# Kernel tuning notes

Hardware: AMD Instinct MI355X
Metric: run time of the kernel (lower is better)

## Reference

```python
import jax, jax.numpy as jnp
import numpy as np

EPSILON = 0.1      # init kwarg epsilon
NUM_STAB = 1e-06   # init kwarg num_stab
B, D, C = 4096, 3072, 10


def setup_inputs() -> dict:
    key = jax.random.key(0)
    k1, k2 = jax.random.split(key)
    data = jax.random.normal(k1, (B, D), dtype=jnp.float32)
    # small scale keeps softmax probs near-uniform -> rho well-conditioned
    W = jax.random.normal(k2, (D, C), dtype=jnp.float32) * 0.02
    return {"data": data, "W": W}


def _probs(logits, c):
    # output = softmax(...) * (1 - c*num_stab) + num_stab  (numerical stabilization)
    p = jax.nn.softmax(logits, axis=-1)
    return p * (1.0 - c * NUM_STAB) + NUM_STAB


def reference(data, W):
    c = W.shape[1]
    m = c - 1

    def g(x):  # x: [D] -> new_output row: [m]
        p = _probs(x @ W, c)
        s = jnp.sqrt(p)
        return 2.0 * s[:m] / (1.0 - s[m])

    # Vectorized Jacobian: replaces the m sequential autograd.grad calls.
    jac = jax.vmap(jax.jacrev(g))(data)            # [B, m, D]

    p = _probs(data @ W, c)                        # [B, C]
    s_m = jnp.sqrt(p[:, m])                        # [B]
    delta = 2.0 * jnp.arccos(jnp.sqrt(p / c).sum(axis=1))   # [B]
    rho = (2.0 * (1.0 - s_m) - p[:, :m].sum(axis=1)) / (1.0 - s_m)  # [B]
    jac_norm = jnp.sqrt(jnp.square(jac).sum(axis=(1, 2)))   # [B] Frobenius norm per sample
    reg = jax.nn.elu(jac_norm - delta / (rho * EPSILON))
    return reg.mean()
```

## Files before the change

### kernel.cpp

```cpp
#include <hip/hip_runtime.h>
#include <math.h>

#define NB 4096
#define ND 3072
#define NC 10
#define NM 9

static constexpr float kEps      = 0.1f;
static constexpr float kNumStab  = 1e-6f;
static constexpr float kAlpha    = 1.0f - (float)NC * kNumStab;
static constexpr float kInvSqrtC = 0.31622776601683794f;


__global__ __launch_bounds__(256) void gram_kernel(
        const float* __restrict__ W, float* __restrict__ G) {
    int e = blockIdx.x, j = 0;
    while (e >= NC - j) { e -= NC - j; ++j; }
    const int k = j + e;
    float acc = 0.0f;
    for (int d = threadIdx.x; d < ND; d += 256)
        acc = fmaf(W[d * NC + j], W[d * NC + k], acc);
    #pragma unroll
    for (int off = 32; off > 0; off >>= 1) acc += __shfl_xor(acc, off, 64);
    __shared__ float part[4];
    if ((threadIdx.x & 63) == 0) part[threadIdx.x >> 6] = acc;
    __syncthreads();
    if (threadIdx.x == 0) {
        const float g = part[0] + part[1] + part[2] + part[3];
        G[j * NC + k] = g;
        G[k * NC + j] = g;
    }
}

__global__ __launch_bounds__(256, 4) void main_kernel(
        const float* __restrict__ data, const float* __restrict__ W,
        const float* __restrict__ G, float* __restrict__ out) {
    __shared__ float Gs[100];
    __shared__ float regs[4];

    const int tid  = threadIdx.x;
    const int lane = tid & 63;
    const int wv   = tid >> 6;

    if (tid < 100) Gs[tid] = G[tid];
    __syncthreads();

    const int s = blockIdx.x * 4 + wv;
    const float4* d4 = reinterpret_cast<const float4*>(data) + (size_t)s * (ND / 4);
    const float4* W4 = reinterpret_cast<const float4*>(W);

    float acc[NC];
    #pragma unroll
    for (int k = 0; k < NC; ++k) acc[k] = 0.0f;

    #pragma unroll 2
    for (int it = 0; it < 12; ++it) {
        const int f = it * 64 + lane;
        const float4 x = d4[f];
        const float4* wp = W4 + (size_t)f * 10;
        float4 wq[10];
        #pragma unroll
        for (int jj = 0; jj < 10; ++jj) wq[jj] = wp[jj];
        const float xs[4] = {x.x, x.y, x.z, x.w};
        #pragma unroll
        for (int jj = 0; jj < 10; ++jj) {
            const int mb = 4 * jj;
            acc[(mb + 0) % 10] = fmaf(xs[(mb + 0) / 10], wq[jj].x, acc[(mb + 0) % 10]);
            acc[(mb + 1) % 10] = fmaf(xs[(mb + 1) / 10], wq[jj].y, acc[(mb + 1) % 10]);
            acc[(mb + 2) % 10] = fmaf(xs[(mb + 2) / 10], wq[jj].z, acc[(mb + 2) % 10]);
            acc[(mb + 3) % 10] = fmaf(xs[(mb + 3) / 10], wq[jj].w, acc[(mb + 3) % 10]);
        }
    }

    #pragma unroll
    for (int k = 0; k < NC; ++k) {
        float v = acc[k];
        #pragma unroll
        for (int off = 32; off > 0; off >>= 1) v += __shfl_xor(v, off, 64);
        acc[k] = v;
    }

    if (lane == 0) {
        float z[NC];
        #pragma unroll
        for (int k = 0; k < NC; ++k) z[k] = acc[k];

        float zm = z[0];
        #pragma unroll
        for (int k = 1; k < NC; ++k) zm = fmaxf(zm, z[k]);
        float e[NC], Zs = 0.0f;
        #pragma unroll
        for (int k = 0; k < NC; ++k) { e[k] = expf(z[k] - zm); Zs += e[k]; }
        const float inv = 1.0f / Zs;

        float sg[NC], p[NC], sq[NC], u[NC];
        #pragma unroll
        for (int k = 0; k < NC; ++k) {
            sg[k] = e[k] * inv;
            p[k]  = kAlpha * sg[k] + kNumStab;
            sq[k] = sqrtf(p[k]);
            u[k]  = sg[k] / sq[k];
        }
        const float qd = 1.0f - sq[NM];

        float v[NC], t = 0.0f;
        #pragma unroll
        for (int k = 0; k < NC; ++k) {
            float a = 0.0f;
            #pragma unroll
            for (int j = 0; j < NC; ++j) a = fmaf(Gs[k * NC + j], sg[j], a);
            v[k] = a;
            t = fmaf(sg[k], a, t);
        }
        const float vM = v[NM], uM = u[NM];
        const float QMM = Gs[NC * NC - 1] - 2.0f * vM + t;

        float sumJ = 0.0f;
        #pragma unroll
        for (int i = 0; i < NM; ++i) {
            const float Qii = Gs[i * NC + i] - 2.0f * v[i] + t;
            const float QiM = Gs[i * NC + NM] - v[i] - vM + t;
            const float r = sq[i] / qd;
            sumJ += u[i] * u[i] * Qii
                  + 2.0f * u[i] * uM * r * QiM
                  + uM * uM * r * r * QMM;
        }
        const float jn = (kAlpha / qd) * sqrtf(fmaxf(sumJ, 0.0f));

        float ssum = 0.0f;
        #pragma unroll
        for (int k = 0; k < NC; ++k) ssum += sq[k];
        const float ac = fminf(1.0f, fmaxf(-1.0f, ssum * kInvSqrtC));
        const float delta = 2.0f * acosf(ac);

        float psum = 0.0f;
        #pragma unroll
        for (int k = 0; k < NM; ++k) psum += p[k];
        const float rho = (2.0f * qd - psum) / qd;

        const float a = jn - delta / (rho * kEps);
        regs[wv] = (a > 0.0f) ? a : expm1f(a);
    }
    __syncthreads();
    if (tid == 0) {
        atomicAdd(out, (regs[0] + regs[1] + regs[2] + regs[3]) * (1.0f / (float)NB));
    }
}

extern "C" void kernel_launch(void* const* d_in, const int* in_sizes, int n_in,
                              void* d_out, int out_size, void* d_ws, size_t ws_size,
                              hipStream_t stream) {
    const float* data = (const float*)d_in[0];
    const float* W    = (const float*)d_in[1];
    float* out = (float*)d_out;
    float* G   = (float*)d_ws;

    hipMemsetAsync(out, 0, sizeof(float), stream);
    gram_kernel<<<(NC * (NC + 1)) / 2, 256, 0, stream>>>(W, G);
    main_kernel<<<NB / 4, 256, 0, stream>>>(data, W, G, out);
}
```

Measured before the change: 115.9 us.

## Transpose W to class-major layout and process two samples per wavefront

Adds a transpose kernel that writes W in class-major float4 layout, so the main and gram kernels read W with coalesced float4 loads instead of 40-byte-strided rows. The main kernel now has each wavefront handle two samples, so every loaded W fragment feeds twice as many FMAs and W traffic per sample is halved. Occupancy hint drops from 4 to 2 blocks per CU, and there is one extra kernel launch and a workspace copy of W.

```diff
diff --git a/kernel.cpp b/kernel.cpp
--- a/kernel.cpp
+++ b/kernel.cpp
@@ -5,6 +5,7 @@
 #define ND 3072
 #define NC 10
 #define NM 9
+#define NF (ND / 4)
 
 static constexpr float kEps      = 0.1f;
 static constexpr float kNumStab  = 1e-6f;
@@ -12,14 +13,32 @@
 static constexpr float kInvSqrtC = 0.31622776601683794f;
 
 
+__global__ __launch_bounds__(256) void transpose_kernel(
+        const float* __restrict__ W, float* __restrict__ Wt) {
+    const int c = blockIdx.x * 256 + threadIdx.x;
+    if (c >= NC * NF) return;
+    const int k = c / NF;
+    const int m = c - k * NF;
+    float4 v;
+    v.x = W[(4 * m + 0) * NC + k];
+    v.y = W[(4 * m + 1) * NC + k];
+    v.z = W[(4 * m + 2) * NC + k];
+    v.w = W[(4 * m + 3) * NC + k];
+    reinterpret_cast<float4*>(Wt)[c] = v;
+}
+
 __global__ __launch_bounds__(256) void gram_kernel(
-        const float* __restrict__ W, float* __restrict__ G) {
+        const float* __restrict__ Wt, float* __restrict__ G) {
     int e = blockIdx.x, j = 0;
     while (e >= NC - j) { e -= NC - j; ++j; }
     const int k = j + e;
+    const float4* a = reinterpret_cast<const float4*>(Wt) + j * NF;
+    const float4* b = reinterpret_cast<const float4*>(Wt) + k * NF;
     float acc = 0.0f;
-    for (int d = threadIdx.x; d < ND; d += 256)
-        acc = fmaf(W[d * NC + j], W[d * NC + k], acc);
+    for (int i = threadIdx.x; i < NF; i += 256) {
+        const float4 av = a[i], bv = b[i];
+        acc += av.x * bv.x + av.y * bv.y + av.z * bv.z + av.w * bv.w;
+    }
     #pragma unroll
     for (int off = 32; off > 0; off >>= 1) acc += __shfl_xor(acc, off, 64);
     __shared__ float part[4];
@@ -32,11 +51,11 @@
     }
 }
 
-__global__ __launch_bounds__(256, 4) void main_kernel(
-        const float* __restrict__ data, const float* __restrict__ W,
+__global__ __launch_bounds__(256, 2) void main_kernel(
+        const float* __restrict__ data, const float* __restrict__ Wt,
         const float* __restrict__ G, float* __restrict__ out) {
     __shared__ float Gs[100];
-    __shared__ float regs[4];
+    __shared__ float regs[8];
 
     const int tid  = threadIdx.x;
     const int lane = tid & 63;
@@ -45,45 +64,52 @@
     if (tid < 100) Gs[tid] = G[tid];
     __syncthreads();
 
-    const int s = blockIdx.x * 4 + wv;
-    const float4* d4 = reinterpret_cast<const float4*>(data) + (size_t)s * (ND / 4);
-    const float4* W4 = reinterpret_cast<const float4*>(W);
+    const int s0 = blockIdx.x * 8 + wv * 2;
+    const float4* d0 = reinterpret_cast<const float4*>(data) + (size_t)s0 * NF;
+    const float4* d1 = d0 + NF;
+    const float4* Wt4 = reinterpret_cast<const float4*>(Wt);
 
-    float acc[NC];
+    float acc[2][NC];
     #pragma unroll
-    for (int k = 0; k < NC; ++k) acc[k] = 0.0f;
+    for (int s = 0; s < 2; ++s)
+        #pragma unroll
+        for (int k = 0; k < NC; ++k) acc[s][k] = 0.0f;
 
     #pragma unroll 2
     for (int it = 0; it < 12; ++it) {
         const int f = it * 64 + lane;
-        const float4 x = d4[f];
-        const float4* wp = W4 + (size_t)f * 10;
-        float4 wq[10];
+        const float4 x0 = d0[f];
+        const float4 x1 = d1[f];
+        float4 wq[NC];
         #pragma unroll
-        for (int jj = 0; jj < 10; ++jj) wq[jj] = wp[jj];
-        const float xs[4] = {x.x, x.y, x.z, x.w};
+        for (int k = 0; k < NC; ++k) wq[k] = Wt4[k * NF + f];
         #pragma unroll
-        for (int jj = 0; jj < 10; ++jj) {
-            const int mb = 4 * jj;
-            acc[(mb + 0) % 10] = fmaf(xs[(mb + 0) / 10], wq[jj].x, acc[(mb + 0) % 10]);
-            acc[(mb + 1) % 10] = fmaf(xs[(mb + 1) / 10], wq[jj].y, acc[(mb + 1) % 10]);
-            acc[(mb + 2) % 10] = fmaf(xs[(mb + 2) / 10], wq[jj].z, acc[(mb + 2) % 10]);
-            acc[(mb + 3) % 10] = fmaf(xs[(mb + 3) / 10], wq[jj].w, acc[(mb + 3) % 10]);
+        for (int k = 0; k < NC; ++k) {
+            acc[0][k] = fmaf(x0.x, wq[k].x, acc[0][k]);
+            acc[0][k] = fmaf(x0.y, wq[k].y, acc[0][k]);
+            acc[0][k] = fmaf(x0.z, wq[k].z, acc[0][k]);
+            acc[0][k] = fmaf(x0.w, wq[k].w, acc[0][k]);
+            acc[1][k] = fmaf(x1.x, wq[k].x, acc[1][k]);
+            acc[1][k] = fmaf(x1.y, wq[k].y, acc[1][k]);
+            acc[1][k] = fmaf(x1.z, wq[k].z, acc[1][k]);
+            acc[1][k] = fmaf(x1.w, wq[k].w, acc[1][k]);
         }
     }
 
     #pragma unroll
-    for (int k = 0; k < NC; ++k) {
-        float v = acc[k];
+    for (int s = 0; s < 2; ++s)
         #pragma unroll
-        for (int off = 32; off > 0; off >>= 1) v += __shfl_xor(v, off, 64);
-        acc[k] = v;
-    }
+        for (int k = 0; k < NC; ++k) {
+            float v = acc[s][k];
+            #pragma unroll
+            for (int off = 32; off > 0; off >>= 1) v += __shfl_xor(v, off, 64);
+            acc[s][k] = v;
+        }
 
-    if (lane == 0) {
+    if (lane < 2) {
         float z[NC];
         #pragma unroll
-        for (int k = 0; k < NC; ++k) z[k] = acc[k];
+        for (int k = 0; k < NC; ++k) z[k] = (lane == 0) ? acc[0][k] : acc[1][k];
 
         float zm = z[0];
         #pragma unroll
@@ -139,11 +165,14 @@
         const float rho = (2.0f * qd - psum) / qd;
 
         const float a = jn - delta / (rho * kEps);
-        regs[wv] = (a > 0.0f) ? a : expm1f(a);
+        regs[wv * 2 + lane] = (a > 0.0f) ? a : expm1f(a);
     }
     __syncthreads();
     if (tid == 0) {
-        atomicAdd(out, (regs[0] + regs[1] + regs[2] + regs[3]) * (1.0f / (float)NB));
+        float bs = 0.0f;
+        #pragma unroll
+        for (int i = 0; i < 8; ++i) bs += regs[i];
+        atomicAdd(out, bs * (1.0f / (float)NB));
     }
 }
 
@@ -153,9 +182,11 @@
     const float* data = (const float*)d_in[0];
     const float* W    = (const float*)d_in[1];
     float* out = (float*)d_out;
-    float* G   = (float*)d_ws;
+    float* Wt  = (float*)d_ws;
+    float* G   = Wt + NC * ND;
 
     hipMemsetAsync(out, 0, sizeof(float), stream);
-    gram_kernel<<<(NC * (NC + 1)) / 2, 256, 0, stream>>>(W, G);
-    main_kernel<<<NB / 4, 256, 0, stream>>>(data, W, G, out);
+    transpose_kernel<<<(NC * NF + 255) / 256, 256, 0, stream>>>(W, Wt);
+    gram_kernel<<<(NC * (NC + 1)) / 2, 256, 0, stream>>>(Wt, G);
+    main_kernel<<<NB / 8, 256, 0, stream>>>(data, Wt, G, out);
 }
```

Measured after the change: 99.46 us. 1.17x faster.
